# Kernel tuning notes

Measured on AMD Instinct MI355X. Metric: run time of the kernel, lower is better.

The kernel has to match this reference:

```python
import jax, jax.numpy as jnp
import numpy as np

B, N, D, R, E = 512, 32, 300, 5, 256
V_SENSE, V_GLOBAL = 20000, 50000  # last_idx_senses, last_idx_globals - last_idx_senses


def setup_inputs() -> dict:
    key = jax.random.key(0)
    ks = jax.random.split(key, 10)
    x = jax.random.normal(ks[0], (B, N, D), jnp.float32)
    edge_index = jax.random.randint(ks[1], (B, 2, E), 0, N)
    edge_type = jnp.sort(jax.random.randint(ks[2], (B, E), 0, R), axis=-1)
    # parameters (xavier-ish scales)
    conv_W = jax.random.normal(ks[3], (R, D, D), jnp.float32) * np.float32(1.0 / np.sqrt(D))
    W0 = jax.random.normal(ks[4], (D, D), jnp.float32) * np.float32(np.sqrt(2.0 / (D + D)))
    update_gate = jnp.ones((1,), jnp.float32)
    glob_W = jax.random.normal(ks[5], (V_GLOBAL, D), jnp.float32) * np.float32(1.0 / np.sqrt(D))
    glob_b = jnp.zeros((V_GLOBAL,), jnp.float32)
    sense_W = jax.random.normal(ks[6], (V_SENSE, D), jnp.float32) * np.float32(1.0 / np.sqrt(D))
    sense_b = jnp.zeros((V_SENSE,), jnp.float32)
    memory0 = jnp.zeros((N, D), jnp.float32)  # initial persisted memory (zeros vector broadcast)
    return dict(x=x, edge_index=edge_index, edge_type=edge_type, conv_W=conv_W, W0=W0,
                update_gate=update_gate, glob_W=glob_W, glob_b=glob_b,
                sense_W=sense_W, sense_b=sense_b, memory0=memory0)


def reference(x, edge_index, edge_type, conv_W, W0, update_gate, glob_W, glob_b, sense_W, sense_b, memory0):
    R_ = conv_W.shape[0]
    N_ = x.shape[1]

    def step(mem, inp):
        xs, ei, et = inp                      # [N,D], [2,E], [E]
        src, dst = ei[0], ei[1]
        # per-relation transformed features (GCNConv, bias=False)
        xw = jnp.einsum('nd,rde->rne', xs, conv_W)          # [R,N,D]
        # per-relation degrees with self-loops (PyG GCNConv symmetric norm)
        onehot = jax.nn.one_hot(et, R_, dtype=xs.dtype)     # [E,R]
        deg = 1.0 + jax.ops.segment_sum(onehot, dst, num_segments=N_)  # [N,R]
        dinv = jax.lax.rsqrt(deg)                           # [N,R]
        coeff = dinv[src, et] * dinv[dst, et]               # [E]
        msg = coeff[:, None] * xw[et, src]                  # [E,D]
        agg = jax.ops.segment_sum(msg, dst, num_segments=N_)  # sum over relations' convs
        self_term = jnp.einsum('rnd,nr->nd', xw, dinv * dinv)  # self-loop of each GCNConv
        composite = agg + self_term
        # prevlayer_connection = eye(N) @ (x @ W_0) = x @ W_0
        proposed = composite + xs @ W0
        new_mem = update_gate * proposed + (1.0 - update_gate) * mem  # rgcn_conv, persisted
        x1 = jax.nn.relu(new_mem)[0]                        # current node features [D]
        return new_mem, x1

    _, x1_all = jax.lax.scan(step, memory0, (x, edge_index, edge_type))  # [B,D]
    logits_g = x1_all @ glob_W.T + glob_b                   # [B,V_GLOBAL]
    logits_s = x1_all @ sense_W.T + sense_b                 # [B,V_SENSE]
    return (jax.nn.log_softmax(logits_g, axis=-1), jax.nn.log_softmax(logits_s, axis=-1))
```

## Files before the change

kernel.cpp:

```cpp
#include <hip/hip_runtime.h>
#include <stdint.h>

#define BDIM   512
#define NNODE  32
#define DDIM   300
#define NREL   5
#define NEDGE  256
#define VGLOB  50000
#define VSENSE 20000

#define K1PAD  1824
#define K2PAD  320
#define TILE_M 128
#define TILE_N 128
#define TILE_K 32
#define TG_GLOB  391
#define TG_SENSE 157
#define GROWS  50048
#define SROWS  20096
#define WROWS  70144
#define NCHUNK 3
#define KCH    19

typedef __attribute__((ext_vector_type(8))) short short8;
typedef __attribute__((ext_vector_type(4))) float f32x4;

__device__ __forceinline__ unsigned short f2bf(float x) {
    unsigned int u = __float_as_uint(x);
    u += 0x7fffu + ((u >> 16) & 1u);
    return (unsigned short)(u >> 16);
}

__device__ __forceinline__ float powi(float x, int n) {
    float r = 1.f, p = x;
    while (n) { if (n & 1) r *= p; p *= p; n >>= 1; }
    return r;
}

__global__ __launch_bounds__(256) void k_prep_z(
    const float* __restrict__ x, const int* __restrict__ ei,
    const int* __restrict__ et, unsigned short* __restrict__ Zb)
{
    int b = blockIdx.x, t = threadIdx.x;
    __shared__ int   cnt[NNODE * NREL];
    __shared__ float dinv[NNODE * NREL];
    __shared__ int   ssrc[NEDGE];
    __shared__ int   sdst[NEDGE];
    __shared__ int   setp[NEDGE];
    __shared__ float z[6][DDIM];

    const int* src = ei + (size_t)b * 2 * NEDGE;
    const int* dst = src + NEDGE;
    const int* etb = et + (size_t)b * NEDGE;

    if (t < NNODE * NREL) cnt[t] = 0;
    __syncthreads();
    if (t < NEDGE) {
        int s = src[t], d = dst[t], r = etb[t];
        ssrc[t] = s; sdst[t] = d; setp[t] = r;
        atomicAdd(&cnt[d * NREL + r], 1);
    }
    __syncthreads();
    if (t < NNODE * NREL) dinv[t] = rsqrtf(1.0f + (float)cnt[t]);
    __syncthreads();

    const float* xb = x + (size_t)b * NNODE * DDIM;
    for (int d = t; d < DDIM; d += 256) {
        float x0 = xb[d];
#pragma unroll
        for (int r = 0; r < NREL; r++) { float c = dinv[r]; z[r][d] = c * c * x0; }
        z[5][d] = x0;
    }
    __syncthreads();
    for (int e = 0; e < NEDGE; e++) {
        if (sdst[e] != 0) continue;
        int s = ssrc[e], r = setp[e];
        float coeff = dinv[s * NREL + r] * dinv[r];
        const float* xs = xb + (size_t)s * DDIM;
        for (int d = t; d < DDIM; d += 256) z[r][d] += coeff * xs[d];
    }
    __syncthreads();
    unsigned short* zo = Zb + (size_t)b * K1PAD;
    for (int k = t; k < K1PAD; k += 256) {
        unsigned short v = 0;
        if (k < 6 * DDIM) { int r = k / DDIM, d = k - r * DDIM; v = f2bf(z[r][d]); }
        zo[k] = v;
    }
}

__global__ __launch_bounds__(256) void k_prep_w(
    const float* __restrict__ convW, const float* __restrict__ W0f,
    unsigned short* __restrict__ Wcb)
{
    int idx = blockIdx.x * 256 + threadIdx.x;
    if (idx >= 384 * K1PAD) return;
    int n = idx / K1PAD, k = idx - n * K1PAD;
    float v = 0.f;
    if (n < DDIM && k < 6 * DDIM) {
        int r = k / DDIM, d = k - r * DDIM;
        v = (r < NREL) ? convW[((size_t)r * DDIM + d) * DDIM + n]
                       : W0f[(size_t)d * DDIM + n];
    }
    Wcb[idx] = f2bf(v);
}

__global__ __launch_bounds__(256) void k_conv_w2(
    const float* __restrict__ globW, const float* __restrict__ senseW,
    unsigned short* __restrict__ Wgb)
{
    int idx = blockIdx.x * 256 + threadIdx.x;
    int row = idx / 80, kq = (idx - row * 80) * 4;
    unsigned int p0 = 0, p1 = 0;
    if (kq < DDIM) {
        const float* srcp = nullptr;
        if (row < GROWS) { if (row < VGLOB) srcp = globW + (size_t)row * DDIM; }
        else { int sr = row - GROWS; if (sr < VSENSE) srcp = senseW + (size_t)sr * DDIM; }
        if (srcp) {
            float4 v = *(const float4*)(srcp + kq);
            p0 = (unsigned int)f2bf(v.x) | ((unsigned int)f2bf(v.y) << 16);
            p1 = (unsigned int)f2bf(v.z) | ((unsigned int)f2bf(v.w) << 16);
        }
    }
    uint2 pp; pp.x = p0; pp.y = p1;
    *(uint2*)(Wgb + (size_t)row * K2PAD + kq) = pp;
}

template<int MODE, bool BF16B>
__global__ __launch_bounds__(256) void k_gemm(
    const unsigned short* __restrict__ A, int ldk, int nk, int kchunk,
    int tiles0,
    const void* __restrict__ B0, int ldb0, int ksrc0, int brows0,
    const float* __restrict__ bias0, float* __restrict__ C0, long ldc0,
    int nstore0, const float* __restrict__ lse0, int tilebase0,
    const void* __restrict__ B1, int ldb1, int ksrc1, int brows1,
    const float* __restrict__ bias1, float* __restrict__ C1, long ldc1,
    int nstore1, const float* __restrict__ lse1, int tilebase1,
    float* __restrict__ pmax, float* __restrict__ psum)
{
    __shared__ __align__(16) short Alds[TILE_M * TILE_K];
    __shared__ __align__(16) short Blds[TILE_N * TILE_K];

    int t = threadIdx.x;
    int bx = blockIdx.x;
    const void* Bsrc; const float *bias, *lse; float* Cout;
    long ldc; int ldb, ksrc, brows, nstore, tileidx;
    if (bx < tiles0) {
        Bsrc = B0; bias = bias0; Cout = C0; lse = lse0; ldc = ldc0;
        ldb = ldb0; ksrc = ksrc0; brows = brows0; nstore = nstore0;
        tileidx = tilebase0 + bx;
    } else {
        bx -= tiles0;
        Bsrc = B1; bias = bias1; Cout = C1; lse = lse1; ldc = ldc1;
        ldb = ldb1; ksrc = ksrc1; brows = brows1; nstore = nstore1;
        tileidx = tilebase1 + bx;
    }
    int n0 = bx * TILE_N;
    int m0 = blockIdx.y * TILE_M;

    int kt_lo = 0, kt_hi = nk / TILE_K;
    if constexpr (MODE == 0) {
        if (kchunk > 0) {
            kt_lo = blockIdx.z * kchunk;
            int hi = kt_lo + kchunk;
            if (hi < kt_hi) kt_hi = hi;
            Cout += (size_t)blockIdx.z * (BDIM * 304);
        }
    }

    int lane = t & 63, wid = t >> 6;
    int wm = wid >> 1, wn = wid & 1;
    int l15 = lane & 15, lq = lane >> 4;

    f32x4 acc[4][4] = {};

    int arow = t >> 1, acol = (t & 1) * 16;
    const unsigned short* aptr = A + (size_t)(m0 + arow) * ldk + acol;
    int brow4 = t >> 2, bk8 = (t & 3) * 8;
    int brow = t >> 3, bkq = (t & 7) * 4;

    for (int kt = kt_lo; kt < kt_hi; ++kt) {
        int k0 = kt * TILE_K;
        uint4 a0 = *(const uint4*)(aptr + k0);
        uint4 a1 = *(const uint4*)(aptr + k0 + 8);
        if constexpr (BF16B) {
            const unsigned short* bb = (const unsigned short*)Bsrc;
            uint4 b0 = *(const uint4*)(bb + (size_t)(n0 + brow4) * ldb + k0 + bk8);
            uint4 b1 = *(const uint4*)(bb + (size_t)(n0 + 64 + brow4) * ldb + k0 + bk8);
            __syncthreads();
            *(uint4*)&Alds[arow * TILE_K + acol] = a0;
            *(uint4*)&Alds[arow * TILE_K + acol + 8] = a1;
            *(uint4*)&Blds[brow4 * TILE_K + bk8] = b0;
            *(uint4*)&Blds[(64 + brow4) * TILE_K + bk8] = b1;
        } else {
            const float* bf = (const float*)Bsrc;
            float4 bv[4];
#pragma unroll
            for (int j = 0; j < 4; j++) {
                int row = n0 + brow + 32 * j;
                float4 v = {0.f, 0.f, 0.f, 0.f};
                if (row < brows && (k0 + bkq + 4) <= ksrc)
                    v = *(const float4*)(bf + (size_t)row * ldb + k0 + bkq);
                bv[j] = v;
            }
            __syncthreads();
            *(uint4*)&Alds[arow * TILE_K + acol] = a0;
            *(uint4*)&Alds[arow * TILE_K + acol + 8] = a1;
#pragma unroll
            for (int j = 0; j < 4; j++) {
                unsigned int p0 = (unsigned int)f2bf(bv[j].x) | ((unsigned int)f2bf(bv[j].y) << 16);
                unsigned int p1 = (unsigned int)f2bf(bv[j].z) | ((unsigned int)f2bf(bv[j].w) << 16);
                uint2 pp; pp.x = p0; pp.y = p1;
                *(uint2*)&Blds[(brow + 32 * j) * TILE_K + bkq] = pp;
            }
        }
        __syncthreads();
        short8 afr[4], bfr[4];
#pragma unroll
        for (int i = 0; i < 4; i++) {
            afr[i] = *(const short8*)&Alds[(wm * 64 + i * 16 + l15) * TILE_K + lq * 8];
            bfr[i] = *(const short8*)&Blds[(wn * 64 + i * 16 + l15) * TILE_K + lq * 8];
        }
#pragma unroll
        for (int mi = 0; mi < 4; mi++)
#pragma unroll
            for (int ni = 0; ni < 4; ni++)
                acc[mi][ni] = __builtin_amdgcn_mfma_f32_16x16x32_bf16(
                    afr[mi], bfr[ni], acc[mi][ni], 0, 0, 0);
    }

    if constexpr (MODE == 1) {
        __shared__ float sMax[128][2];
        __shared__ float sSum[128][2];
#pragma unroll
        for (int mi = 0; mi < 4; mi++) {
#pragma unroll
            for (int r = 0; r < 4; r++) {
                float vals[4];
                float rowmax = -3.0e38f;
#pragma unroll
                for (int ni = 0; ni < 4; ni++) {
                    int col = n0 + wn * 64 + ni * 16 + l15;
                    float v = -3.0e38f;
                    if (col < nstore) v = acc[mi][ni][r] + bias[col];
                    vals[ni] = v;
                    rowmax = fmaxf(rowmax, v);
                }
#pragma unroll
                for (int off = 1; off < 16; off <<= 1)
                    rowmax = fmaxf(rowmax, __shfl_xor(rowmax, off, 64));
                float s = 0.f;
#pragma unroll
                for (int ni = 0; ni < 4; ni++) s += __expf(vals[ni] - rowmax);
#pragma unroll
                for (int off = 1; off < 16; off <<= 1) s += __shfl_xor(s, off, 64);
                if (l15 == 0) {
                    int rl = wm * 64 + mi * 16 + lq * 4 + r;
                    sMax[rl][wn] = rowmax; sSum[rl][wn] = s;
                }
            }
        }
        __syncthreads();
        if (t < 128) {
            float ma = sMax[t][0], mb = sMax[t][1];
            float M = fmaxf(ma, mb);
            float S = sSum[t][0] * __expf(ma - M) + sSum[t][1] * __expf(mb - M);
            size_t o = (size_t)tileidx * BDIM + (m0 + t);
            pmax[o] = M; psum[o] = S;
        }
    } else {
#pragma unroll
        for (int mi = 0; mi < 4; mi++) {
            int row = m0 + wm * 64 + mi * 16 + lq * 4;
#pragma unroll
            for (int ni = 0; ni < 4; ni++) {
                int col = n0 + wn * 64 + ni * 16 + l15;
                if (col < nstore) {
#pragma unroll
                    for (int r = 0; r < 4; r++) {
                        float v = acc[mi][ni][r];
                        if constexpr (MODE == 2) v += bias[col] - lse[row + r];
                        Cout[(size_t)(row + r) * ldc + col] = v;
                    }
                }
            }
        }
    }
}

__global__ __launch_bounds__(320) void k_scan_local(
    const float* __restrict__ prop, float* __restrict__ scanA,
    const float* __restrict__ gate)
{
    int d = threadIdx.x; if (d >= 304) return;
    int blk = blockIdx.x;
    float g = gate[0], og = 1.f - g;
    float m = 0.f;
    const float* p0 = prop + (size_t)blk * 64 * 304 + d;
    const float* p1 = p0 + (size_t)BDIM * 304;
    const float* p2 = p1 + (size_t)BDIM * 304;
    float* o = scanA + (size_t)blk * 64 * 304 + d;
#pragma unroll
    for (int i = 0; i < 64; i++) {
        size_t off = (size_t)i * 304;
        float pv = p0[off] + p1[off] + p2[off];
        m = g * pv + og * m;
        o[off] = m;
    }
}

__global__ __launch_bounds__(320) void k_scan_combine(
    const float* __restrict__ scanA, const float* __restrict__ gate,
    const float* __restrict__ mem0, float* __restrict__ mstart)
{
    int d = threadIdx.x; if (d >= DDIM) return;
    float g = gate[0], og = 1.f - g;
    float c64 = powi(og, 64);
    float m = mem0[d];
#pragma unroll
    for (int blk = 0; blk < 8; blk++) {
        mstart[blk * 304 + d] = m;
        m = scanA[(size_t)(blk * 64 + 63) * 304 + d] + c64 * m;
    }
}

__global__ __launch_bounds__(320) void k_finalize_x1(
    const float* __restrict__ scanA, const float* __restrict__ mstart,
    const float* __restrict__ gate, unsigned short* __restrict__ x1b)
{
    int b = blockIdx.x, d = threadIdx.x;
    unsigned short v = 0;
    if (d < DDIM) {
        float g = gate[0], og = 1.f - g;
        float mval = scanA[(size_t)b * 304 + d]
                   + powi(og, (b & 63) + 1) * mstart[(b >> 6) * 304 + d];
        v = f2bf(fmaxf(mval, 0.f));
    }
    if (d < K2PAD) x1b[(size_t)b * K2PAD + d] = v;
}

__global__ __launch_bounds__(256) void k_lse_par(
    const float* __restrict__ pmax, const float* __restrict__ psum,
    float* __restrict__ lse)
{
    int b = blockIdx.x, seg = blockIdx.y, t = threadIdx.x;
    int base = seg ? TG_GLOB : 0;
    int nt = seg ? TG_SENSE : TG_GLOB;
    float M = -3.0e38f, S = 0.f;
    for (int i = t; i < nt; i += 256) {
        size_t o = (size_t)(base + i) * BDIM + b;
        float m = pmax[o], s = psum[o];
        if (m > M) { S = S * __expf(M - m) + s; M = m; }
        else       { S += s * __expf(m - M); }
    }
#pragma unroll
    for (int off = 1; off < 64; off <<= 1) {
        float Mo = __shfl_xor(M, off, 64), So = __shfl_xor(S, off, 64);
        float Mn = fmaxf(M, Mo);
        S = S * __expf(M - Mn) + So * __expf(Mo - Mn);
        M = Mn;
    }
    __shared__ float sM[4], sS[4];
    int lane = t & 63, wid = t >> 6;
    if (lane == 0) { sM[wid] = M; sS[wid] = S; }
    __syncthreads();
    if (t == 0) {
        M = sM[0]; S = sS[0];
#pragma unroll
        for (int w = 1; w < 4; w++) {
            float Mo = sM[w], So = sS[w];
            float Mn = fmaxf(M, Mo);
            S = S * __expf(M - Mn) + So * __expf(Mo - Mn);
            M = Mn;
        }
        lse[seg * BDIM + b] = M + __logf(S);
    }
}

extern "C" void kernel_launch(void* const* d_in, const int* in_sizes, int n_in,
                              void* d_out, int out_size, void* d_ws, size_t ws_size,
                              hipStream_t stream)
{
    (void)in_sizes; (void)n_in; (void)out_size;
    const float* x      = (const float*)d_in[0];
    const int*   ei     = (const int*)d_in[1];
    const int*   et     = (const int*)d_in[2];
    const float* convW  = (const float*)d_in[3];
    const float* W0f    = (const float*)d_in[4];
    const float* gate   = (const float*)d_in[5];
    const float* globW  = (const float*)d_in[6];
    const float* globB  = (const float*)d_in[7];
    const float* senseW = (const float*)d_in[8];
    const float* senseB = (const float*)d_in[9];
    const float* mem0   = (const float*)d_in[10];
    float* out = (float*)d_out;

    char* w = (char*)d_ws;
    unsigned short* Zb  = (unsigned short*)(w + 0);
    unsigned short* Wcb = (unsigned short*)(w + 1867776);
    unsigned short* x1b = (unsigned short*)(w + 3268608);
    float* prop         = (float*)(w + 3596288);
    float* scanA        = (float*)(w + 5464064);
    float* mstart       = (float*)(w + 6086656);
    float* pmax         = (float*)(w + 6096384);
    float* psum         = (float*)(w + 7218688);
    float* lse          = (float*)(w + 8340992);
    unsigned short* Wgb = (unsigned short*)(w + 8345088);
    const size_t WS_NEED_BIG = 8345088 + (size_t)WROWS * K2PAD * 2;
    bool bigws = ws_size >= WS_NEED_BIG;

    k_prep_z<<<BDIM, 256, 0, stream>>>(x, ei, et, Zb);
    k_prep_w<<<(384 * K1PAD + 255) / 256, 256, 0, stream>>>(convW, W0f, Wcb);
    if (bigws)
        k_conv_w2<<<(WROWS * 80) / 256, 256, 0, stream>>>(globW, senseW, Wgb);

    k_gemm<0, true><<<dim3(3, 4, NCHUNK), 256, 0, stream>>>(Zb, K1PAD, K1PAD, KCH,
        3, Wcb, K1PAD, K1PAD, 384, nullptr, prop, 304, 304, nullptr, 0,
        nullptr, 0, 0, 0, nullptr, nullptr, 0, 0, nullptr, 0,
        nullptr, nullptr);

    k_scan_local<<<8, 320, 0, stream>>>(prop, scanA, gate);
    k_scan_combine<<<1, 320, 0, stream>>>(scanA, gate, mem0, mstart);
    k_finalize_x1<<<BDIM, 320, 0, stream>>>(scanA, mstart, gate, x1b);

    if (bigws) {
        const unsigned short* WgbS = Wgb + (size_t)GROWS * K2PAD;
        k_gemm<1, true><<<dim3(TG_GLOB + TG_SENSE, 4), 256, 0, stream>>>(x1b, K2PAD, K2PAD, 0,
            TG_GLOB, Wgb, K2PAD, K2PAD, GROWS, globB, nullptr, 0, VGLOB, nullptr, 0,
            WgbS, K2PAD, K2PAD, SROWS, senseB, nullptr, 0, VSENSE, nullptr, TG_GLOB,
            pmax, psum);
        k_lse_par<<<dim3(BDIM, 2), 256, 0, stream>>>(pmax, psum, lse);
        k_gemm<2, true><<<dim3(TG_GLOB + TG_SENSE, 4), 256, 0, stream>>>(x1b, K2PAD, K2PAD, 0,
            TG_GLOB, Wgb, K2PAD, K2PAD, GROWS, globB, out, VGLOB, VGLOB, lse, 0,
            WgbS, K2PAD, K2PAD, SROWS, senseB, out + (size_t)BDIM * VGLOB, VSENSE, VSENSE, lse + BDIM, 0,
            nullptr, nullptr);
    } else {
        k_gemm<1, false><<<dim3(TG_GLOB + TG_SENSE, 4), 256, 0, stream>>>(x1b, K2PAD, K2PAD, 0,
            TG_GLOB, globW, DDIM, DDIM, VGLOB, globB, nullptr, 0, VGLOB, nullptr, 0,
            senseW, DDIM, DDIM, VSENSE, senseB, nullptr, 0, VSENSE, nullptr, TG_GLOB,
            pmax, psum);
        k_lse_par<<<dim3(BDIM, 2), 256, 0, stream>>>(pmax, psum, lse);
        k_gemm<2, false><<<dim3(TG_GLOB + TG_SENSE, 4), 256, 0, stream>>>(x1b, K2PAD, K2PAD, 0,
            TG_GLOB, globW, DDIM, DDIM, VGLOB, globB, out, VGLOB, VGLOB, lse, 0,
            senseW, DDIM, DDIM, VSENSE, senseB, out + (size_t)BDIM * VGLOB, VSENSE, VSENSE, lse + BDIM, 0,
            nullptr, nullptr);
    }
}
```

Before: 425.7 us.

## Use direct global-to-LDS loads with K=64 swizzled tiles and grouped tile order

Rewrites the bf16 GEMM to load A and B tiles straight into LDS with global_load_lds, using 64-wide K steps and an XOR swizzle to avoid bank conflicts. K1PAD is padded to a multiple of 64 so the first GEMM fits. Blocks of the vocab GEMMs are remapped so groups of 8 N-tiles share all 4 M-tiles, which improves L2 reuse of the weights. The scan is also split into 16 chunks of 32 rows for more parallelism. The cost is more LDS per block and an ordering that depends on exact tile counts.

New measurement: 391.2 us. 8.1% less time.

```diff
diff --git a/kernel.cpp b/kernel.cpp
--- a/kernel.cpp
+++ b/kernel.cpp
@@ -9,18 +9,18 @@
 #define VGLOB  50000
 #define VSENSE 20000
 
-#define K1PAD  1824
+#define K1PAD  1856
 #define K2PAD  320
-#define TILE_M 128
-#define TILE_N 128
-#define TILE_K 32
 #define TG_GLOB  391
 #define TG_SENSE 157
+#define TGTOT  548
 #define GROWS  50048
 #define SROWS  20096
 #define WROWS  70144
 #define NCHUNK 3
-#define KCH    19
+#define KCH    10
+#define NSCH   16
+#define SCHL   32
 
 typedef __attribute__((ext_vector_type(8))) short short8;
 typedef __attribute__((ext_vector_type(4))) float f32x4;
@@ -35,6 +35,12 @@
     float r = 1.f, p = x;
     while (n) { if (n & 1) r *= p; p *= p; n >>= 1; }
     return r;
+}
+
+#define AS1 __attribute__((address_space(1)))
+#define AS3 __attribute__((address_space(3)))
+__device__ __forceinline__ void gload16(const void* gp, void* lp) {
+    __builtin_amdgcn_global_load_lds((AS1 void*)gp, (AS3 void*)lp, 16, 0, 0);
 }
 
 __global__ __launch_bounds__(256) void k_prep_z(
@@ -125,24 +131,183 @@
     *(uint2*)(Wgb + (size_t)row * K2PAD + kq) = pp;
 }
 
-template<int MODE, bool BF16B>
-__global__ __launch_bounds__(256) void k_gemm(
+template<int MODE>
+__global__ __launch_bounds__(256) void k_gemm_b(
     const unsigned short* __restrict__ A, int ldk, int nk, int kchunk,
     int tiles0,
-    const void* __restrict__ B0, int ldb0, int ksrc0, int brows0,
+    const unsigned short* __restrict__ B0, int ldb0,
     const float* __restrict__ bias0, float* __restrict__ C0, long ldc0,
     int nstore0, const float* __restrict__ lse0, int tilebase0,
-    const void* __restrict__ B1, int ldb1, int ksrc1, int brows1,
+    const unsigned short* __restrict__ B1, int ldb1,
     const float* __restrict__ bias1, float* __restrict__ C1, long ldc1,
     int nstore1, const float* __restrict__ lse1, int tilebase1,
     float* __restrict__ pmax, float* __restrict__ psum)
 {
-    __shared__ __align__(16) short Alds[TILE_M * TILE_K];
-    __shared__ __align__(16) short Blds[TILE_N * TILE_K];
+    __shared__ __align__(16) char Alds[128 * 128];
+    __shared__ __align__(16) char Blds[128 * 128];
+
+    int t = threadIdx.x;
+    int tile, mrep;
+    if constexpr (MODE == 0) {
+        tile = blockIdx.x; mrep = blockIdx.y;
+    } else {
+        int i = blockIdx.x + TGTOT * blockIdx.y;
+        if (i < 2176) { int g = i >> 5, r = i & 31; tile = g * 8 + (r & 7); mrep = r >> 3; }
+        else          { int j = i - 2176; tile = 544 + (j & 3); mrep = j >> 2; }
+    }
+
+    const unsigned short* Bp; const float *bias, *lse; float* Cout;
+    long ldc; int ldb, nstore, tileidx, tloc;
+    if (tile < tiles0) {
+        Bp = B0; bias = bias0; Cout = C0; lse = lse0; ldc = ldc0;
+        ldb = ldb0; nstore = nstore0; tloc = tile; tileidx = tilebase0 + tile;
+    } else {
+        tloc = tile - tiles0;
+        Bp = B1; bias = bias1; Cout = C1; lse = lse1; ldc = ldc1;
+        ldb = ldb1; nstore = nstore1; tileidx = tilebase1 + tloc;
+    }
+    int n0 = tloc * 128;
+    int m0 = mrep * 128;
+
+    int kt_lo = 0, kt_hi = nk >> 6;
+    if constexpr (MODE == 0) {
+        if (kchunk > 0) {
+            kt_lo = blockIdx.z * kchunk;
+            int hi = kt_lo + kchunk;
+            if (hi < kt_hi) kt_hi = hi;
+            Cout += (size_t)blockIdx.z * (BDIM * 304);
+        }
+    }
+
+    int lane = t & 63, wid = t >> 6;
+    int wm = wid >> 1, wn = wid & 1;
+    int l15 = lane & 15, lq = lane >> 4;
+
+    int trow = t >> 3;
+    int sb = ((t & 7) << 4) ^ ((trow & 7) << 4);
+    const char* Ag = (const char*)A + (size_t)(m0 + trow) * (ldk * 2) + sb;
+    const char* Bg = (const char*)Bp + (size_t)(n0 + trow) * (ldb * 2) + sb;
+    char* Al = Alds + t * 16;
+    char* Bl = Blds + t * 16;
+    size_t a32 = (size_t)32 * (ldk * 2);
+    size_t b32 = (size_t)32 * (ldb * 2);
+
+    int sw = (l15 & 7) << 4;
+    int aoff0 = (lq * 16) ^ sw;
+    int aoff1 = (64 + lq * 16) ^ sw;
+    const char* Arow = Alds + (wm * 64 + l15) * 128;
+    const char* Brow = Blds + (wn * 64 + l15) * 128;
+
+    f32x4 acc[4][4] = {};
+
+    for (int kt = kt_lo; kt < kt_hi; ++kt) {
+        int k0b = kt << 7;
+        const char* Agk = Ag + k0b;
+        const char* Bgk = Bg + k0b;
+#pragma unroll
+        for (int c = 0; c < 4; c++) {
+            gload16(Agk + c * a32, Al + c * 4096);
+            gload16(Bgk + c * b32, Bl + c * 4096);
+        }
+        __syncthreads();
+        short8 afr[4][2], bfr[4][2];
+#pragma unroll
+        for (int i = 0; i < 4; i++) {
+            const char* Ab = Arow + i * (16 * 128);
+            const char* Bb = Brow + i * (16 * 128);
+            afr[i][0] = *(const short8*)(Ab + aoff0);
+            afr[i][1] = *(const short8*)(Ab + aoff1);
+            bfr[i][0] = *(const short8*)(Bb + aoff0);
+            bfr[i][1] = *(const short8*)(Bb + aoff1);
+        }
+#pragma unroll
+        for (int ks = 0; ks < 2; ks++)
+#pragma unroll
+            for (int mi = 0; mi < 4; mi++)
+#pragma unroll
+                for (int ni = 0; ni < 4; ni++)
+                    acc[mi][ni] = __builtin_amdgcn_mfma_f32_16x16x32_bf16(
+                        afr[mi][ks], bfr[ni][ks], acc[mi][ni], 0, 0, 0);
+        __syncthreads();
+    }
+
+    if constexpr (MODE == 1) {
+        __shared__ float sMax[128][2];
+        __shared__ float sSum[128][2];
+#pragma unroll
+        for (int mi = 0; mi < 4; mi++) {
+#pragma unroll
+            for (int r = 0; r < 4; r++) {
+                float vals[4];
+                float rowmax = -3.0e38f;
+#pragma unroll
+                for (int ni = 0; ni < 4; ni++) {
+                    int col = n0 + wn * 64 + ni * 16 + l15;
+                    float v = -3.0e38f;
+                    if (col < nstore) v = acc[mi][ni][r] + bias[col];
+                    vals[ni] = v;
+                    rowmax = fmaxf(rowmax, v);
+                }
+#pragma unroll
+                for (int off = 1; off < 16; off <<= 1)
+                    rowmax = fmaxf(rowmax, __shfl_xor(rowmax, off, 64));
+                float s = 0.f;
+#pragma unroll
+                for (int ni = 0; ni < 4; ni++) s += __expf(vals[ni] - rowmax);
+#pragma unroll
+                for (int off = 1; off < 16; off <<= 1) s += __shfl_xor(s, off, 64);
+                if (l15 == 0) {
+                    int rl = wm * 64 + mi * 16 + lq * 4 + r;
+                    sMax[rl][wn] = rowmax; sSum[rl][wn] = s;
+                }
+            }
+        }
+        __syncthreads();
+        if (t < 128) {
+            float ma = sMax[t][0], mb = sMax[t][1];
+            float M = fmaxf(ma, mb);
+            float S = sSum[t][0] * __expf(ma - M) + sSum[t][1] * __expf(mb - M);
+            size_t o = (size_t)tileidx * BDIM + (m0 + t);
+            pmax[o] = M; psum[o] = S;
+        }
+    } else {
+#pragma unroll
+        for (int mi = 0; mi < 4; mi++) {
+            int row = m0 + wm * 64 + mi * 16 + lq * 4;
+#pragma unroll
+            for (int ni = 0; ni < 4; ni++) {
+                int col = n0 + wn * 64 + ni * 16 + l15;
+                if (col < nstore) {
+#pragma unroll
+                    for (int r = 0; r < 4; r++) {
+                        float v = acc[mi][ni][r];
+                        if constexpr (MODE == 2) v += bias[col] - lse[row + r];
+                        Cout[(size_t)(row + r) * ldc + col] = v;
+                    }
+                }
+            }
+        }
+    }
+}
+
+template<int MODE>
+__global__ __launch_bounds__(256) void k_gemm_f32(
+    const unsigned short* __restrict__ A, int ldk, int nk,
+    int tiles0,
+    const float* __restrict__ B0, int ldb0, int ksrc0, int brows0,
+    const float* __restrict__ bias0, float* __restrict__ C0, long ldc0,
+    int nstore0, const float* __restrict__ lse0, int tilebase0,
+    const float* __restrict__ B1, int ldb1, int ksrc1, int brows1,
+    const float* __restrict__ bias1, float* __restrict__ C1, long ldc1,
+    int nstore1, const float* __restrict__ lse1, int tilebase1,
+    float* __restrict__ pmax, float* __restrict__ psum)
+{
+    __shared__ __align__(16) short Alds[128 * 32];
+    __shared__ __align__(16) short Blds[128 * 32];
 
     int t = threadIdx.x;
     int bx = blockIdx.x;
-    const void* Bsrc; const float *bias, *lse; float* Cout;
+    const float* Bsrc; const float *bias, *lse; float* Cout;
     long ldc; int ldb, ksrc, brows, nstore, tileidx;
     if (bx < tiles0) {
         Bsrc = B0; bias = bias0; Cout = C0; lse = lse0; ldc = ldc0;
@@ -154,18 +319,8 @@
         ldb = ldb1; ksrc = ksrc1; brows = brows1; nstore = nstore1;
         tileidx = tilebase1 + bx;
     }
-    int n0 = bx * TILE_N;
-    int m0 = blockIdx.y * TILE_M;
-
-    int kt_lo = 0, kt_hi = nk / TILE_K;
-    if constexpr (MODE == 0) {
-        if (kchunk > 0) {
-            kt_lo = blockIdx.z * kchunk;
-            int hi = kt_lo + kchunk;
-            if (hi < kt_hi) kt_hi = hi;
-            Cout += (size_t)blockIdx.z * (BDIM * 304);
-        }
-    }
+    int n0 = bx * 128;
+    int m0 = blockIdx.y * 128;
 
     int lane = t & 63, wid = t >> 6;
     int wm = wid >> 1, wn = wid & 1;
@@ -175,50 +330,38 @@
 
     int arow = t >> 1, acol = (t & 1) * 16;
     const unsigned short* aptr = A + (size_t)(m0 + arow) * ldk + acol;
-    int brow4 = t >> 2, bk8 = (t & 3) * 8;
     int brow = t >> 3, bkq = (t & 7) * 4;
 
-    for (int kt = kt_lo; kt < kt_hi; ++kt) {
-        int k0 = kt * TILE_K;
+    int kt_hi = nk / 32;
+    for (int kt = 0; kt < kt_hi; ++kt) {
+        int k0 = kt * 32;
         uint4 a0 = *(const uint4*)(aptr + k0);
         uint4 a1 = *(const uint4*)(aptr + k0 + 8);
-        if constexpr (BF16B) {
-            const unsigned short* bb = (const unsigned short*)Bsrc;
-            uint4 b0 = *(const uint4*)(bb + (size_t)(n0 + brow4) * ldb + k0 + bk8);
-            uint4 b1 = *(const uint4*)(bb + (size_t)(n0 + 64 + brow4) * ldb + k0 + bk8);
-            __syncthreads();
-            *(uint4*)&Alds[arow * TILE_K + acol] = a0;
-            *(uint4*)&Alds[arow * TILE_K + acol + 8] = a1;
-            *(uint4*)&Blds[brow4 * TILE_K + bk8] = b0;
-            *(uint4*)&Blds[(64 + brow4) * TILE_K + bk8] = b1;
-        } else {
-            const float* bf = (const float*)Bsrc;
-            float4 bv[4];
-#pragma unroll
-            for (int j = 0; j < 4; j++) {
-                int row = n0 + brow + 32 * j;
-                float4 v = {0.f, 0.f, 0.f, 0.f};
-                if (row < brows && (k0 + bkq + 4) <= ksrc)
-                    v = *(const float4*)(bf + (size_t)row * ldb + k0 + bkq);
-                bv[j] = v;
-            }
-            __syncthreads();
-            *(uint4*)&Alds[arow * TILE_K + acol] = a0;
-            *(uint4*)&Alds[arow * TILE_K + acol + 8] = a1;
-#pragma unroll
-            for (int j = 0; j < 4; j++) {
-                unsigned int p0 = (unsigned int)f2bf(bv[j].x) | ((unsigned int)f2bf(bv[j].y) << 16);
-                unsigned int p1 = (unsigned int)f2bf(bv[j].z) | ((unsigned int)f2bf(bv[j].w) << 16);
-                uint2 pp; pp.x = p0; pp.y = p1;
-                *(uint2*)&Blds[(brow + 32 * j) * TILE_K + bkq] = pp;
-            }
+        float4 bv[4];
+#pragma unroll
+        for (int j = 0; j < 4; j++) {
+            int row = n0 + brow + 32 * j;
+            float4 v = {0.f, 0.f, 0.f, 0.f};
+            if (row < brows && (k0 + bkq + 4) <= ksrc)
+                v = *(const float4*)(Bsrc + (size_t)row * ldb + k0 + bkq);
+            bv[j] = v;
+        }
+        __syncthreads();
+        *(uint4*)&Alds[arow * 32 + acol] = a0;
+        *(uint4*)&Alds[arow * 32 + acol + 8] = a1;
+#pragma unroll
+        for (int j = 0; j < 4; j++) {
+            unsigned int p0 = (unsigned int)f2bf(bv[j].x) | ((unsigned int)f2bf(bv[j].y) << 16);
+            unsigned int p1 = (unsigned int)f2bf(bv[j].z) | ((unsigned int)f2bf(bv[j].w) << 16);
+            uint2 pp; pp.x = p0; pp.y = p1;
+            *(uint2*)&Blds[(brow + 32 * j) * 32 + bkq] = pp;
         }
         __syncthreads();
         short8 afr[4], bfr[4];
 #pragma unroll
         for (int i = 0; i < 4; i++) {
-            afr[i] = *(const short8*)&Alds[(wm * 64 + i * 16 + l15) * TILE_K + lq * 8];
-            bfr[i] = *(const short8*)&Blds[(wn * 64 + i * 16 + l15) * TILE_K + lq * 8];
+            afr[i] = *(const short8*)&Alds[(wm * 64 + i * 16 + l15) * 32 + lq * 8];
+            bfr[i] = *(const short8*)&Blds[(wn * 64 + i * 16 + l15) * 32 + lq * 8];
         }
 #pragma unroll
         for (int mi = 0; mi < 4; mi++)
@@ -295,12 +438,12 @@
     int blk = blockIdx.x;
     float g = gate[0], og = 1.f - g;
     float m = 0.f;
-    const float* p0 = prop + (size_t)blk * 64 * 304 + d;
+    const float* p0 = prop + (size_t)blk * SCHL * 304 + d;
     const float* p1 = p0 + (size_t)BDIM * 304;
     const float* p2 = p1 + (size_t)BDIM * 304;
-    float* o = scanA + (size_t)blk * 64 * 304 + d;
-#pragma unroll
-    for (int i = 0; i < 64; i++) {
+    float* o = scanA + (size_t)blk * SCHL * 304 + d;
+#pragma unroll
+    for (int i = 0; i < SCHL; i++) {
         size_t off = (size_t)i * 304;
         float pv = p0[off] + p1[off] + p2[off];
         m = g * pv + og * m;
@@ -314,12 +457,12 @@
 {
     int d = threadIdx.x; if (d >= DDIM) return;
     float g = gate[0], og = 1.f - g;
-    float c64 = powi(og, 64);
+    float cS = powi(og, SCHL);
     float m = mem0[d];
 #pragma unroll
-    for (int blk = 0; blk < 8; blk++) {
+    for (int blk = 0; blk < NSCH; blk++) {
         mstart[blk * 304 + d] = m;
-        m = scanA[(size_t)(blk * 64 + 63) * 304 + d] + c64 * m;
+        m = scanA[(size_t)(blk * SCHL + SCHL - 1) * 304 + d] + cS * m;
     }
 }
 
@@ -332,7 +475,7 @@
     if (d < DDIM) {
         float g = gate[0], og = 1.f - g;
         float mval = scanA[(size_t)b * 304 + d]
-                   + powi(og, (b & 63) + 1) * mstart[(b >> 6) * 304 + d];
+                   + powi(og, (b & (SCHL - 1)) + 1) * mstart[(b >> 5) * 304 + d];
         v = f2bf(fmaxf(mval, 0.f));
     }
     if (d < K2PAD) x1b[(size_t)b * K2PAD + d] = v;
@@ -396,16 +539,16 @@
 
     char* w = (char*)d_ws;
     unsigned short* Zb  = (unsigned short*)(w + 0);
-    unsigned short* Wcb = (unsigned short*)(w + 1867776);
-    unsigned short* x1b = (unsigned short*)(w + 3268608);
-    float* prop         = (float*)(w + 3596288);
-    float* scanA        = (float*)(w + 5464064);
-    float* mstart       = (float*)(w + 6086656);
-    float* pmax         = (float*)(w + 6096384);
-    float* psum         = (float*)(w + 7218688);
-    float* lse          = (float*)(w + 8340992);
-    unsigned short* Wgb = (unsigned short*)(w + 8345088);
-    const size_t WS_NEED_BIG = 8345088 + (size_t)WROWS * K2PAD * 2;
+    unsigned short* Wcb = (unsigned short*)(w + 1900544);
+    unsigned short* x1b = (unsigned short*)(w + 3325952);
+    float* prop         = (float*)(w + 3653632);
+    float* scanA        = (float*)(w + 5521408);
+    float* mstart       = (float*)(w + 6144000);
+    float* pmax         = (float*)(w + 6163456);
+    float* psum         = (float*)(w + 7285760);
+    float* lse          = (float*)(w + 8408064);
+    unsigned short* Wgb = (unsigned short*)(w + 8412160);
+    const size_t WS_NEED_BIG = 8412160 + (size_t)WROWS * K2PAD * 2;
     bool bigws = ws_size >= WS_NEED_BIG;
 
     k_prep_z<<<BDIM, 256, 0, stream>>>(x, ei, et, Zb);
@@ -413,33 +556,33 @@
     if (bigws)
         k_conv_w2<<<(WROWS * 80) / 256, 256, 0, stream>>>(globW, senseW, Wgb);
 
-    k_gemm<0, true><<<dim3(3, 4, NCHUNK), 256, 0, stream>>>(Zb, K1PAD, K1PAD, KCH,
-        3, Wcb, K1PAD, K1PAD, 384, nullptr, prop, 304, 304, nullptr, 0,
-        nullptr, 0, 0, 0, nullptr, nullptr, 0, 0, nullptr, 0,
+    k_gemm_b<0><<<dim3(3, 4, NCHUNK), 256, 0, stream>>>(Zb, K1PAD, K1PAD, KCH,
+        3, Wcb, K1PAD, nullptr, prop, 304, 304, nullptr, 0,
+        nullptr, 0, nullptr, nullptr, 0, 0, nullptr, 0,
         nullptr, nullptr);
 
-    k_scan_local<<<8, 320, 0, stream>>>(prop, scanA, gate);
+    k_scan_local<<<NSCH, 320, 0, stream>>>(prop, scanA, gate);
     k_scan_combine<<<1, 320, 0, stream>>>(scanA, gate, mem0, mstart);
     k_finalize_x1<<<BDIM, 320, 0, stream>>>(scanA, mstart, gate, x1b);
 
     if (bigws) {
         const unsigned short* WgbS = Wgb + (size_t)GROWS * K2PAD;
-        k_gemm<1, true><<<dim3(TG_GLOB + TG_SENSE, 4), 256, 0, stream>>>(x1b, K2PAD, K2PAD, 0,
-            TG_GLOB, Wgb, K2PAD, K2PAD, GROWS, globB, nullptr, 0, VGLOB, nullptr, 0,
-            WgbS, K2PAD, K2PAD, SROWS, senseB, nullptr, 0, VSENSE, nullptr, TG_GLOB,
+        k_gemm_b<1><<<dim3(TGTOT, 4), 256, 0, stream>>>(x1b, K2PAD, K2PAD, 0,
+            TG_GLOB, Wgb, K2PAD, globB, nullptr, 0, VGLOB, nullptr, 0,
+            WgbS, K2PAD, senseB, nullptr, 0, VSENSE, nullptr, TG_GLOB,
             pmax, psum);
         k_lse_par<<<dim3(BDIM, 2), 256, 0, stream>>>(pmax, psum, lse);
-        k_gemm<2, true><<<dim3(TG_GLOB + TG_SENSE, 4), 256, 0, stream>>>(x1b, K2PAD, K2PAD, 0,
-            TG_GLOB, Wgb, K2PAD, K2PAD, GROWS, globB, out, VGLOB, VGLOB, lse, 0,
-            WgbS, K2PAD, K2PAD, SROWS, senseB, out + (size_t)BDIM * VGLOB, VSENSE, VSENSE, lse + BDIM, 0,
+        k_gemm_b<2><<<dim3(TGTOT, 4), 256, 0, stream>>>(x1b, K2PAD, K2PAD, 0,
+            TG_GLOB, Wgb, K2PAD, globB, out, VGLOB, VGLOB, lse, 0,
+            WgbS, K2PAD, senseB, out + (size_t)BDIM * VGLOB, VSENSE, VSENSE, lse + BDIM, 0,
             nullptr, nullptr);
     } else {
-        k_gemm<1, false><<<dim3(TG_GLOB + TG_SENSE, 4), 256, 0, stream>>>(x1b, K2PAD, K2PAD, 0,
+        k_gemm_f32<1><<<dim3(TGTOT, 4), 256, 0, stream>>>(x1b, K2PAD, K2PAD,
             TG_GLOB, globW, DDIM, DDIM, VGLOB, globB, nullptr, 0, VGLOB, nullptr, 0,
             senseW, DDIM, DDIM, VSENSE, senseB, nullptr, 0, VSENSE, nullptr, TG_GLOB,
             pmax, psum);
         k_lse_par<<<dim3(BDIM, 2), 256, 0, stream>>>(pmax, psum, lse);
-        k_gemm<2, false><<<dim3(TG_GLOB + TG_SENSE, 4), 256, 0, stream>>>(x1b, K2PAD, K2PAD, 0,
+        k_gemm_f32<2><<<dim3(TGTOT, 4), 256, 0, stream>>>(x1b, K2PAD, K2PAD,
             TG_GLOB, globW, DDIM, DDIM, VGLOB, globB, out, VGLOB, VGLOB, lse, 0,
             senseW, DDIM, DDIM, VSENSE, senseB, out + (size_t)BDIM * VGLOB, VSENSE, VSENSE, lse + BDIM, 0,
             nullptr, nullptr);
```
